# Optimization experiments

Hardware: AMD Instinct MI355X
Metric: run time of the kernel (lower is better)

## Reference

```python
import jax, jax.numpy as jnp
from jax import lax
import numpy as np

NUM_LABELS = 48
BATCH, SEQ_LEN = 512, 1024


def setup_inputs() -> dict:
    key = jax.random.key(0)
    k1, k2, k3, k4, k5 = jax.random.split(key, 5)
    emissions = jax.random.normal(k1, (BATCH, SEQ_LEN, NUM_LABELS), dtype=jnp.float32)
    labels = jax.random.randint(k2, (BATCH, SEQ_LEN), 0, NUM_LABELS, dtype=jnp.int32)
    mask = jnp.ones((BATCH, SEQ_LEN), dtype=jnp.int32)
    transitions = jax.random.normal(k3, (NUM_LABELS, NUM_LABELS), dtype=jnp.float32)
    start_transitions = jax.random.normal(k4, (NUM_LABELS,), dtype=jnp.float32)
    end_transitions = jax.random.normal(k5, (NUM_LABELS,), dtype=jnp.float32)
    return {
        "emissions": emissions,
        "labels": labels,
        "mask": mask,
        "transitions": transitions,
        "start_transitions": start_transitions,
        "end_transitions": end_transitions,
    }


def _gold_score(emissions, labels, mask, transitions, start_transitions, end_transitions):
    maskf = mask.astype(emissions.dtype)
    # emissions gathered at gold labels: (B, T)
    emit = jnp.take_along_axis(emissions, labels[..., None], axis=2)[..., 0]
    # NOTE: original indexes transitions[labels_t, labels_{t-1}] (cur, prev)
    trans = transitions[labels[:, 1:], labels[:, :-1]]  # (B, T-1)
    lengths = jnp.sum(mask, axis=1) - 1  # index of last real token
    last_labels = jnp.take_along_axis(labels, lengths[:, None], axis=1)[:, 0]
    score = (start_transitions[labels[:, 0]] + emit[:, 0]
             + jnp.sum((emit[:, 1:] + trans) * maskf[:, 1:], axis=1)
             + end_transitions[last_labels])
    return score  # (B,)


def _forward_algorithm(emissions, mask, transitions, start_transitions, end_transitions):
    # carry: alpha scores (B, L)
    score0 = start_transitions[None, :] + emissions[:, 0]

    def step(score, xs):
        emit_t, mask_t = xs  # (B, L), (B,)
        # logsumexp over previous label i of score[b,i] + transitions[i,j]
        next_score = jax.nn.logsumexp(score[:, :, None] + transitions[None, :, :], axis=1) + emit_t
        score = jnp.where(mask_t[:, None].astype(bool), next_score, score)
        return score, None

    xs = (jnp.moveaxis(emissions[:, 1:], 1, 0), jnp.moveaxis(mask[:, 1:], 1, 0))
    score, _ = lax.scan(step, score0, xs)
    return jax.nn.logsumexp(score + end_transitions[None, :], axis=1)  # (B,)


def reference(emissions, labels, mask, transitions, start_transitions, end_transitions):
    gold = _gold_score(emissions, labels, mask, transitions, start_transitions, end_transitions)
    fwd = _forward_algorithm(emissions, mask, transitions, start_transitions, end_transitions)
    return jnp.mean(fwd - gold)
```

## Files before the change

### kernel.cpp

```cpp
#include <hip/hip_runtime.h>

constexpr int NL    = 48;
constexpr int SEQ   = 1024;
constexpr int BATCH = 512;

__device__ __forceinline__ float lane_bcast(float v, int lane) {
    return __int_as_float(__builtin_amdgcn_readlane(__float_as_int(v), lane));
}

#define CRF_STEP(T_, SLOT_) do {                                              \
    float ee_ = __expf(embuf[SLOT_]);                                         \
    int   mt_ = mbuf[SLOT_];                                                  \
    int   tn_ = (T_) + 8; if (tn_ > SEQ - 1) tn_ = SEQ - 1;                   \
    embuf[SLOT_] = em[tn_ * NL + jc];                                         \
    mbuf[SLOT_]  = mk[tn_];                                                   \
    float a0_ = 0.f, a1_ = 0.f, a2_ = 0.f, a3_ = 0.f;                         \
    _Pragma("unroll")                                                         \
    for (int i_ = 0; i_ < NL; i_ += 4) {                                      \
        a0_ = fmaf(lane_bcast(v, i_ + 0), Ec[i_ + 0], a0_);                   \
        a1_ = fmaf(lane_bcast(v, i_ + 1), Ec[i_ + 1], a1_);                   \
        a2_ = fmaf(lane_bcast(v, i_ + 2), Ec[i_ + 2], a2_);                   \
        a3_ = fmaf(lane_bcast(v, i_ + 3), Ec[i_ + 3], a3_);                   \
    }                                                                         \
    float acc_ = (a0_ + a1_) + (a2_ + a3_);                                   \
    v = mt_ ? acc_ * ee_ : v;                                                 \
} while (0)

#define CRF_RENORM do {                                                       \
    float m_ = v;                                                             \
    _Pragma("unroll")                                                         \
    for (int o_ = 32; o_; o_ >>= 1) m_ = fmaxf(m_, __shfl_xor(m_, o_));       \
    float r_ = 1.0f / m_;                                                     \
    v *= r_;                                                                  \
    S += __logf(m_);                                                          \
} while (0)

__global__ __launch_bounds__(128, 1) void crf_fused(
    const float* __restrict__ emissions, const int* __restrict__ labels,
    const int* __restrict__ mask, const float* __restrict__ trans,
    const float* __restrict__ startt, const float* __restrict__ endt,
    float* __restrict__ gold_out, float* __restrict__ fwd_out)
{
    const int b = blockIdx.x;
    const int tid = threadIdx.x;
    const float* em = emissions + (size_t)b * SEQ * NL;
    const int*   mk = mask + b * SEQ;

    if (tid < 64) {
        const int  j   = tid;
        const bool act = (j < NL);
        const int  jc  = act ? j : NL - 1;

        float Ec[NL];
        #pragma unroll
        for (int i = 0; i < NL; ++i) {
            float t = trans[i * NL + jc];
            Ec[i] = act ? __expf(t) : 0.0f;
        }

        float s0 = act ? (startt[jc] + em[jc]) : -3.0e38f;
        float m0 = s0;
        #pragma unroll
        for (int o = 32; o; o >>= 1) m0 = fmaxf(m0, __shfl_xor(m0, o));
        float v = act ? __expf(s0 - m0) : 0.0f;
        float S = m0;

        float embuf[8]; int mbuf[8];
        #pragma unroll
        for (int t = 1; t <= 8; ++t) { embuf[t & 7] = em[t * NL + jc]; mbuf[t & 7] = mk[t]; }

        CRF_STEP(1, 1); CRF_STEP(2, 2); CRF_STEP(3, 3); CRF_STEP(4, 4);
        CRF_RENORM;
        CRF_STEP(5, 5); CRF_STEP(6, 6); CRF_STEP(7, 7);

        for (int tb = 8; tb <= SEQ - 8; tb += 8) {
            CRF_STEP(tb + 0, 0);
            CRF_RENORM;
            CRF_STEP(tb + 1, 1); CRF_STEP(tb + 2, 2); CRF_STEP(tb + 3, 3); CRF_STEP(tb + 4, 4);
            CRF_RENORM;
            CRF_STEP(tb + 5, 5); CRF_STEP(tb + 6, 6); CRF_STEP(tb + 7, 7);
        }

        float w = act ? v * __expf(endt[jc]) : 0.0f;
        #pragma unroll
        for (int o = 32; o; o >>= 1) w += __shfl_xor(w, o);
        if (j == 0) fwd_out[b] = S + __logf(w);
    } else {
        const int l = tid - 64;
        const int* lb = labels + b * SEQ;

        float part = 0.0f; int mcnt = 0;
        for (int t = l; t < SEQ; t += 64) {
            int lt = lb[t];
            int mt = mk[t];
            mcnt += mt;
            if (t == 0) {
                part += startt[lt] + em[lt];
            } else {
                float e  = em[t * NL + lt];
                float tr = trans[lt * NL + lb[t - 1]];
                if (mt) part += e + tr;
            }
        }
        #pragma unroll
        for (int o = 32; o; o >>= 1) {
            part += __shfl_xor(part, o);
            mcnt += __shfl_xor(mcnt, o);
        }
        if (l == 0) {
            int len = mcnt - 1;
            gold_out[b] = part + endt[lb[len]];
        }
    }
}

__global__ __launch_bounds__(64) void crf_reduce(
    const float* __restrict__ gold, const float* __restrict__ fwd,
    float* __restrict__ out)
{
    const int l = threadIdx.x;
    float s = 0.0f;
    for (int bIdx = l; bIdx < BATCH; bIdx += 64) s += fwd[bIdx] - gold[bIdx];
    #pragma unroll
    for (int o = 32; o; o >>= 1) s += __shfl_xor(s, o);
    if (l == 0) out[0] = s * (1.0f / (float)BATCH);
}

extern "C" void kernel_launch(void* const* d_in, const int* in_sizes, int n_in,
                              void* d_out, int out_size, void* d_ws, size_t ws_size,
                              hipStream_t stream) {
    const float* emissions = (const float*)d_in[0];
    const int*   labels    = (const int*)d_in[1];
    const int*   mask      = (const int*)d_in[2];
    const float* trans     = (const float*)d_in[3];
    const float* startt    = (const float*)d_in[4];
    const float* endt      = (const float*)d_in[5];
    float*       out       = (float*)d_out;
    float*       wsf       = (float*)d_ws;

    crf_fused<<<BATCH, 128, 0, stream>>>(emissions, labels, mask, trans, startt, endt,
                                         wsf, wsf + BATCH);
    crf_reduce<<<1, 64, 0, stream>>>(wsf, wsf + BATCH, out);
}
```

Before: 399.0 us.

## Broadcast CRF alpha via LDS float4 reads and fold renorm max into step

Each forward step now writes the alpha vector to shared memory and reads it back as 12 float4 broadcasts, instead of issuing 48 readlane broadcasts. The periodic renormalisation no longer uses a shuffle-xor max reduction. It takes the max from the same LDS values already loaded for the matrix-vector product and scales the new alpha with a fast reciprocal. This targets the serial per-step latency of the lane-broadcast chain and of the six-hop shuffle reduction. In exchange it relies on in-order LDS visibility within a single wavefront, with no barrier, and scales by the previous step's max rather than the current one.

```diff
diff --git a/kernel.cpp b/kernel.cpp
--- a/kernel.cpp
+++ b/kernel.cpp
@@ -4,35 +4,41 @@
 constexpr int SEQ   = 1024;
 constexpr int BATCH = 512;
 
-__device__ __forceinline__ float lane_bcast(float v, int lane) {
-    return __int_as_float(__builtin_amdgcn_readlane(__float_as_int(v), lane));
-}
-
-#define CRF_STEP(T_, SLOT_) do {                                              \
+#define CRF_STEP(T_, SLOT_, RN_) do {                                         \
     float ee_ = __expf(embuf[SLOT_]);                                         \
     int   mt_ = mbuf[SLOT_];                                                  \
     int   tn_ = (T_) + 8; if (tn_ > SEQ - 1) tn_ = SEQ - 1;                   \
     embuf[SLOT_] = em[tn_ * NL + jc];                                         \
     mbuf[SLOT_]  = mk[tn_];                                                   \
-    float a0_ = 0.f, a1_ = 0.f, a2_ = 0.f, a3_ = 0.f;                         \
+    float2 c0_={0.f,0.f}, c1_={0.f,0.f}, c2_={0.f,0.f}, c3_={0.f,0.f};        \
+    float2 mx_={0.f,0.f};                                                     \
     _Pragma("unroll")                                                         \
-    for (int i_ = 0; i_ < NL; i_ += 4) {                                      \
-        a0_ = fmaf(lane_bcast(v, i_ + 0), Ec[i_ + 0], a0_);                   \
-        a1_ = fmaf(lane_bcast(v, i_ + 1), Ec[i_ + 1], a1_);                   \
-        a2_ = fmaf(lane_bcast(v, i_ + 2), Ec[i_ + 2], a2_);                   \
-        a3_ = fmaf(lane_bcast(v, i_ + 3), Ec[i_ + 3], a3_);                   \
+    for (int r_ = 0; r_ < 12; ++r_) {                                         \
+        float4 q_  = vb4[r_];                                                 \
+        float2 eA_ = Ec2[2*r_], eB_ = Ec2[2*r_+1];                            \
+        if (RN_) {                                                            \
+            mx_.x = fmaxf(mx_.x, fmaxf(q_.x, q_.z));                          \
+            mx_.y = fmaxf(mx_.y, fmaxf(q_.y, q_.w));                          \
+        }                                                                     \
+        if (r_ & 1) {                                                         \
+            c2_.x = fmaf(q_.x, eA_.x, c2_.x); c2_.y = fmaf(q_.y, eA_.y, c2_.y);\
+            c3_.x = fmaf(q_.z, eB_.x, c3_.x); c3_.y = fmaf(q_.w, eB_.y, c3_.y);\
+        } else {                                                              \
+            c0_.x = fmaf(q_.x, eA_.x, c0_.x); c0_.y = fmaf(q_.y, eA_.y, c0_.y);\
+            c1_.x = fmaf(q_.z, eB_.x, c1_.x); c1_.y = fmaf(q_.w, eB_.y, c1_.y);\
+        }                                                                     \
     }                                                                         \
-    float acc_ = (a0_ + a1_) + (a2_ + a3_);                                   \
-    v = mt_ ? acc_ * ee_ : v;                                                 \
-} while (0)
-
-#define CRF_RENORM do {                                                       \
-    float m_ = v;                                                             \
-    _Pragma("unroll")                                                         \
-    for (int o_ = 32; o_; o_ >>= 1) m_ = fmaxf(m_, __shfl_xor(m_, o_));       \
-    float r_ = 1.0f / m_;                                                     \
-    v *= r_;                                                                  \
-    S += __logf(m_);                                                          \
+    float2 d0_ = {c0_.x + c2_.x, c0_.y + c2_.y};                              \
+    float2 d1_ = {c1_.x + c3_.x, c1_.y + c3_.y};                              \
+    float acc_ = (d0_.x + d0_.y) + (d1_.x + d1_.y);                           \
+    float nv_  = mt_ ? acc_ * ee_ : v;                                        \
+    if (RN_) {                                                                \
+        float m_ = fmaxf(fmaxf(mx_.x, mx_.y), 1e-30f);                        \
+        nv_ *= __builtin_amdgcn_rcpf(m_);                                     \
+        S += __logf(m_);                                                      \
+    }                                                                         \
+    v = nv_;                                                                  \
+    vb[jc] = v;                                                               \
 } while (0)
 
 __global__ __launch_bounds__(128, 1) void crf_fused(
@@ -41,7 +47,8 @@
     const float* __restrict__ startt, const float* __restrict__ endt,
     float* __restrict__ gold_out, float* __restrict__ fwd_out)
 {
-    const int b = blockIdx.x;
+    __shared__ float4 vb4[12];
+    const int b   = blockIdx.x;
     const int tid = threadIdx.x;
     const float* em = emissions + (size_t)b * SEQ * NL;
     const int*   mk = mask + b * SEQ;
@@ -50,35 +57,36 @@
         const int  j   = tid;
         const bool act = (j < NL);
         const int  jc  = act ? j : NL - 1;
+        float* vb = (float*)vb4;
 
-        float Ec[NL];
+        float2 Ec2[24];
         #pragma unroll
-        for (int i = 0; i < NL; ++i) {
-            float t = trans[i * NL + jc];
-            Ec[i] = act ? __expf(t) : 0.0f;
+        for (int p = 0; p < 24; ++p) {
+            Ec2[p].x = __expf(trans[(2*p)     * NL + jc]);
+            Ec2[p].y = __expf(trans[(2*p + 1) * NL + jc]);
         }
 
-        float s0 = act ? (startt[jc] + em[jc]) : -3.0e38f;
+        float s0 = startt[jc] + em[jc];
         float m0 = s0;
         #pragma unroll
         for (int o = 32; o; o >>= 1) m0 = fmaxf(m0, __shfl_xor(m0, o));
-        float v = act ? __expf(s0 - m0) : 0.0f;
+        float v = __expf(s0 - m0);
         float S = m0;
+        vb[jc] = v;
 
         float embuf[8]; int mbuf[8];
         #pragma unroll
         for (int t = 1; t <= 8; ++t) { embuf[t & 7] = em[t * NL + jc]; mbuf[t & 7] = mk[t]; }
 
-        CRF_STEP(1, 1); CRF_STEP(2, 2); CRF_STEP(3, 3); CRF_STEP(4, 4);
-        CRF_RENORM;
-        CRF_STEP(5, 5); CRF_STEP(6, 6); CRF_STEP(7, 7);
+        CRF_STEP(1, 1, 0); CRF_STEP(2, 2, 0); CRF_STEP(3, 3, 0);
+        CRF_STEP(4, 4, 1);
+        CRF_STEP(5, 5, 0); CRF_STEP(6, 6, 0); CRF_STEP(7, 7, 0);
 
         for (int tb = 8; tb <= SEQ - 8; tb += 8) {
-            CRF_STEP(tb + 0, 0);
-            CRF_RENORM;
-            CRF_STEP(tb + 1, 1); CRF_STEP(tb + 2, 2); CRF_STEP(tb + 3, 3); CRF_STEP(tb + 4, 4);
-            CRF_RENORM;
-            CRF_STEP(tb + 5, 5); CRF_STEP(tb + 6, 6); CRF_STEP(tb + 7, 7);
+            CRF_STEP(tb + 0, 0, 1);
+            CRF_STEP(tb + 1, 1, 0); CRF_STEP(tb + 2, 2, 0); CRF_STEP(tb + 3, 3, 0);
+            CRF_STEP(tb + 4, 4, 1);
+            CRF_STEP(tb + 5, 5, 0); CRF_STEP(tb + 6, 6, 0); CRF_STEP(tb + 7, 7, 0);
         }
 
         float w = act ? v * __expf(endt[jc]) : 0.0f;
```

After: 596.4 us. +49.5%, slower.
